# Kernel optimization log

Measured on AMD Instinct MI355X. Metric: run time of the kernel, lower is better.

The kernel has to match this reference:

```python
import jax, jax.numpy as jnp
import numpy as np

N_NODES = 100000
N_EDGES = 3200000
F_IN = 512
HIDDEN = 16
N_CLASSES = 32
DROPOUT = 0.5


def setup_inputs() -> dict:
    key = jax.random.key(0)
    k1, k2, k3, k4, k5, k6 = jax.random.split(key, 6)
    X = jax.random.normal(k1, (N_NODES, F_IN), dtype=jnp.float32)
    edge_src = jax.random.randint(k2, (N_EDGES,), 0, N_NODES, dtype=jnp.int32)
    edge_dst = jax.random.randint(k3, (N_EDGES,), 0, N_NODES, dtype=jnp.int32)
    # normalized adjacency values (positive, like D^-1/2 A D^-1/2 entries)
    edge_w = jax.random.uniform(k4, (N_EDGES,), dtype=jnp.float32)
    W1 = jax.random.normal(k5, (F_IN, HIDDEN), dtype=jnp.float32) * (1.0 / np.sqrt(F_IN))
    W2 = jax.random.normal(k6, (HIDDEN, N_CLASSES), dtype=jnp.float32) * (1.0 / np.sqrt(HIDDEN))
    return {"X": X, "edge_src": edge_src, "edge_dst": edge_dst,
            "edge_w": edge_w, "W1": W1, "W2": W2}


def _dropout(x, key, rate):
    keep = 1.0 - rate
    mask = jax.random.bernoulli(key, keep, x.shape)
    return jnp.where(mask, x / keep, jnp.zeros((), x.dtype))


def _spmm(h, edge_src, edge_dst, edge_w):
    # A @ h with A given as COO edge list: out[d] = sum_e w_e * h[s_e]
    msgs = h[edge_src] * edge_w[:, None]  # [E, C]
    return jax.ops.segment_sum(msgs, edge_dst, num_segments=h.shape[0])


def reference(X, edge_src, edge_dst, edge_w, W1, W2):
    key = jax.random.key(42)
    kd1, kd2 = jax.random.split(key)
    # layer 1: dropout -> GraphConv(relu)  (Spektral: act(A @ (X @ W)))
    H = _dropout(X, kd1, DROPOUT)
    H = H @ W1                                  # [N, HIDDEN]
    H = _spmm(H, edge_src, edge_dst, edge_w)    # [N, HIDDEN]
    H = jax.nn.relu(H)
    # layer 2: dropout -> GraphConv(softmax)
    H = _dropout(H, kd2, DROPOUT)
    H = H @ W2                                  # [N, N_CLASSES]
    H = _spmm(H, edge_src, edge_dst, edge_w)
    return jax.nn.softmax(H, axis=-1)
```

## Files before the change

### kernel.cpp

```cpp
#include <hip/hip_runtime.h>
#include <stdint.h>
#include <stddef.h>

#define N_NODES   100000
#define N_EDGES   3200000
#define F_IN      512
#define HIDDEN    16
#define N_CLASSES 32

#define BSHIFT 6
#define NBUK   ((N_NODES + 63) >> 6)
#define CAP    2368
#define TILE   8192
#define NB_BIN ((N_EDGES + TILE - 1) / TILE)
#define NW_MASK ((N_NODES * F_IN) / 32)
#define NB_MSK (NW_MASK / 256)
#define NB_G1  ((N_NODES + 63) / 64)

__host__ __device__ __forceinline__ uint32_t rotl32(uint32_t x, int r) {
#ifdef __HIP_DEVICE_COMPILE__
  return __builtin_amdgcn_alignbit(x, x, (uint32_t)(32 - r));
#else
  return (x << r) | (x >> (32 - r));
#endif
}

__host__ __device__ __forceinline__ void tf2x32_full(uint32_t k0, uint32_t k1,
                                                     uint32_t x0, uint32_t x1,
                                                     uint32_t* o0, uint32_t* o1) {
  const uint32_t k2 = k0 ^ k1 ^ 0x1BD11BDAu;
  x0 += k0; x1 += k1;
#define TF_R(r) { x0 += x1; x1 = rotl32(x1, (r)); x1 ^= x0; }
  TF_R(13) TF_R(15) TF_R(26) TF_R(6)   x0 += k1; x1 += k2 + 1u;
  TF_R(17) TF_R(29) TF_R(16) TF_R(24)  x0 += k2; x1 += k0 + 2u;
  TF_R(13) TF_R(15) TF_R(26) TF_R(6)   x0 += k0; x1 += k1 + 3u;
  TF_R(17) TF_R(29) TF_R(16) TF_R(24)  x0 += k1; x1 += k2 + 4u;
  TF_R(13) TF_R(15) TF_R(26) TF_R(6)   x0 += k2; x1 += k0 + 5u;
#undef TF_R
  *o0 = x0; *o1 = x1;
}

__device__ __forceinline__ bool keep_bit(uint32_t k0, uint32_t k1, uint32_t ctr) {
  uint32_t o0, o1;
  tf2x32_full(k0, k1, 0u, ctr, &o0, &o1);
  return (int32_t)(o0 ^ o1) >= 0;
}

__launch_bounds__(256)
__global__ void bin_mask_fused(const int* __restrict__ src, const int* __restrict__ dst,
                               const float* __restrict__ w, int* __restrict__ gcur,
                               int2* __restrict__ ep, uint32_t* __restrict__ mask1,
                               uint32_t kd0, uint32_t kd1) {
  __shared__ int lh[NBUK];
  __shared__ int gb[NBUK];
  const int tid = threadIdx.x;

  if (blockIdx.x < NB_BIN) {
    const int base = blockIdx.x * TILE;
    const int n = min(TILE, N_EDGES - base);

    for (int i = tid; i < NBUK; i += 256) lh[i] = 0;
    __syncthreads();

    for (int i = tid; i < n; i += 256)
      atomicAdd(&lh[dst[base + i] >> BSHIFT], 1);
    __syncthreads();

    for (int b = tid; b < NBUK; b += 256) {
      const int h = lh[b];
      gb[b] = h ? atomicAdd(&gcur[b], h) : 0;
      lh[b] = 0;
    }
    __syncthreads();

    for (int i = tid; i < n; i += 256) {
      const int e = base + i;
      const int d = dst[e];
      const int b = d >> BSHIFT;
      const int pos = gb[b] + atomicAdd(&lh[b], 1);
      if (pos < CAP)
        ep[(size_t)b * CAP + pos] =
            make_int2(src[e] | ((d & 63) << 17), __float_as_int(w[e]));
    }
    return;
  }

  const int mt = (blockIdx.x - NB_BIN) * 256 + tid;
  if (mt < NW_MASK) {
    const uint32_t base = (uint32_t)mt * 32u;
    uint32_t word = 0u;
#pragma unroll
    for (int j = 0; j < 32; j++) {
      uint32_t o0, o1;
      tf2x32_full(kd0, kd1, 0u, base + (uint32_t)j, &o0, &o1);
      word |= ((~(o0 ^ o1)) >> 31) << j;
    }
    mask1[mt] = word;
  }
}

__launch_bounds__(256)
__global__ void gemm1_mask(const float* __restrict__ X,
                           const float* __restrict__ W1,
                           const uint32_t* __restrict__ mask1,
                           float* __restrict__ H1) {
  __shared__ float W1s[F_IN * HIDDEN];
  const int tid = threadIdx.x;
  for (int i = tid; i < (F_IN * HIDDEN) / 4; i += 256) {
    const int f = i >> 2, m = i & 3;
    ((float4*)W1s)[f * 4 + (m ^ ((f >> 2) & 3))] = ((const float4*)W1)[i];
  }
  __syncthreads();

  const int p = tid & 3;
  const int node = blockIdx.x * 64 + (tid >> 2);
  if (node >= N_NODES) return;

  float acc[16];
#pragma unroll
  for (int j = 0; j < 16; j++) acc[j] = 0.0f;

  const float4* Xrow4 = (const float4*)(X + (size_t)node * F_IN);
  const uint32_t* Mrow = mask1 + (size_t)node * 16;
  const int sh0 = p << 2;
  const int sh1 = 16 + (p << 2);

  for (int it2 = 0; it2 < 16; ++it2) {
    const uint32_t mword = Mrow[it2];
    const float4 xv0 = Xrow4[it2 * 8 + p];
    const float4 xv1 = Xrow4[it2 * 8 + 4 + p];
    const uint32_t nib0 = mword >> sh0;
    const uint32_t nib1 = mword >> sh1;
    const float xs0[4] = {xv0.x, xv0.y, xv0.z, xv0.w};
    const float xs1[4] = {xv1.x, xv1.y, xv1.z, xv1.w};

#pragma unroll
    for (int e = 0; e < 4; e++) {
      const float xd = (nib0 >> e) & 1u ? xs0[e] + xs0[e] : 0.0f;
      const int f = it2 * 32 + p * 4 + e;
      const float4* row = (const float4*)&W1s[f * 16];
#pragma unroll
      for (int q = 0; q < 4; q++) {
        const float4 wv = row[q ^ p];
        acc[q * 4 + 0] += xd * wv.x;
        acc[q * 4 + 1] += xd * wv.y;
        acc[q * 4 + 2] += xd * wv.z;
        acc[q * 4 + 3] += xd * wv.w;
      }
    }
#pragma unroll
    for (int e = 0; e < 4; e++) {
      const float xd = (nib1 >> e) & 1u ? xs1[e] + xs1[e] : 0.0f;
      const int f = it2 * 32 + 16 + p * 4 + e;
      const float4* row = (const float4*)&W1s[f * 16];
#pragma unroll
      for (int q = 0; q < 4; q++) {
        const float4 wv = row[q ^ p];
        acc[q * 4 + 0] += xd * wv.x;
        acc[q * 4 + 1] += xd * wv.y;
        acc[q * 4 + 2] += xd * wv.z;
        acc[q * 4 + 3] += xd * wv.w;
      }
    }
  }

  float a2[8];
#pragma unroll
  for (int k = 0; k < 8; k++) {
    const float keep = (p & 2) ? acc[8 + k] : acc[k];
    const float send = (p & 2) ? acc[k]     : acc[8 + k];
    a2[k] = keep + __shfl_xor(send, 2);
  }
  float r0, r1, r2, r3;
  {
    const float k0v = (p & 1) ? a2[4] : a2[0];
    const float s0v = (p & 1) ? a2[0] : a2[4];
    r0 = k0v + __shfl_xor(s0v, 1);
    const float k1v = (p & 1) ? a2[5] : a2[1];
    const float s1v = (p & 1) ? a2[1] : a2[5];
    r1 = k1v + __shfl_xor(s1v, 1);
    const float k2v = (p & 1) ? a2[6] : a2[2];
    const float s2v = (p & 1) ? a2[2] : a2[6];
    r2 = k2v + __shfl_xor(s2v, 1);
    const float k3v = (p & 1) ? a2[7] : a2[3];
    const float s3v = (p & 1) ? a2[3] : a2[7];
    r3 = k3v + __shfl_xor(s3v, 1);
  }
  *(float4*)(H1 + (size_t)node * HIDDEN + p * 4) = make_float4(r0, r1, r2, r3);
}

__launch_bounds__(256)
__global__ void bucket_gather1(const int* __restrict__ gcur, const int2* __restrict__ ep,
                               const float* __restrict__ H1, float* __restrict__ H2d,
                               uint32_t k0, uint32_t k1) {
  __shared__ int2 B[CAP];
  __shared__ int lh[64], lex[64], lcur[64];
  const int tid = threadIdx.x;
  const int b = blockIdx.x;

  if (tid < 64) lh[tid] = 0;
  __syncthreads();

  const int c = min(gcur[b], CAP);
  const int2* ebase = ep + (size_t)b * CAP;

  for (int k = tid; k < c; k += 256)
    atomicAdd(&lh[(ebase[k].x >> 17) & 63], 1);
  __syncthreads();

  if (tid < 64) {
    const int v = lh[tid];
    int s = v;
    for (int off = 1; off < 64; off <<= 1) {
      const int t = __shfl_up(s, off);
      if (tid >= off) s += t;
    }
    lex[tid] = s - v;
    lcur[tid] = s - v;
  }
  __syncthreads();

  for (int k = tid; k < c; k += 256) {
    const int2 r = ebase[k];
    const int p = atomicAdd(&lcur[(r.x >> 17) & 63], 1);
    B[p] = r;
  }
  __syncthreads();

  const int lane = tid & 63, wid = tid >> 6;
  const int ei = lane >> 4, f = lane & 15;
  for (int ln = wid; ln < 64; ln += 4) {
    const int ng = (b << BSHIFT) + ln;
    if (ng >= N_NODES) break;
    const int beg = lex[ln], cnt = lh[ln];
    float acc = 0.0f;
    for (int k = beg + ei; k < beg + cnt; k += 4) {
      const int2 r = B[k];
      acc += __int_as_float(r.y) * H1[(size_t)(r.x & 0x1FFFF) * HIDDEN + f];
    }
    acc += __shfl_xor(acc, 16);
    acc += __shfl_xor(acc, 32);
    float v = fmaxf(acc, 0.0f);
    v = keep_bit(k0, k1, (uint32_t)ng * HIDDEN + (uint32_t)f) ? v * 2.0f : 0.0f;
    if (lane < 16) H2d[(size_t)ng * HIDDEN + f] = v;
  }
}

__launch_bounds__(256)
__global__ void bucket_gather2(const int* __restrict__ gcur, const int2* __restrict__ ep,
                               const float* __restrict__ H2d, const float* __restrict__ W2,
                               float* __restrict__ O) {
  __shared__ int2 B[CAP];
  __shared__ float W2s[HIDDEN][N_CLASSES];
  __shared__ int lh[64], lex[64], lcur[64];
  const int tid = threadIdx.x;
  const int b = blockIdx.x;

  if (tid < 64) lh[tid] = 0;
  for (int i = tid; i < HIDDEN * N_CLASSES; i += 256) ((float*)W2s)[i] = W2[i];
  __syncthreads();

  const int c = min(gcur[b], CAP);
  const int2* ebase = ep + (size_t)b * CAP;

  for (int k = tid; k < c; k += 256)
    atomicAdd(&lh[(ebase[k].x >> 17) & 63], 1);
  __syncthreads();

  if (tid < 64) {
    const int v = lh[tid];
    int s = v;
    for (int off = 1; off < 64; off <<= 1) {
      const int t = __shfl_up(s, off);
      if (tid >= off) s += t;
    }
    lex[tid] = s - v;
    lcur[tid] = s - v;
  }
  __syncthreads();

  for (int k = tid; k < c; k += 256) {
    const int2 r = ebase[k];
    const int p = atomicAdd(&lcur[(r.x >> 17) & 63], 1);
    B[p] = r;
  }
  __syncthreads();

  const int lane = tid & 63, wid = tid >> 6;
  const int ei = lane >> 4, f = lane & 15;
  const int cl = lane & 31;
  for (int ln = wid; ln < 64; ln += 4) {
    const int ng = (b << BSHIFT) + ln;
    if (ng >= N_NODES) break;
    const int beg = lex[ln], cnt = lh[ln];
    float acc = 0.0f;
    for (int k = beg + ei; k < beg + cnt; k += 4) {
      const int2 r = B[k];
      acc += __int_as_float(r.y) * H2d[(size_t)(r.x & 0x1FFFF) * HIDDEN + f];
    }
    acc += __shfl_xor(acc, 16);
    acc += __shfl_xor(acc, 32);
    float lg = 0.0f;
#pragma unroll
    for (int fq = 0; fq < HIDDEN; fq++)
      lg += __shfl(acc, fq) * W2s[fq][cl];
    float m = lg;
#pragma unroll
    for (int off = 16; off >= 1; off >>= 1) m = fmaxf(m, __shfl_xor(m, off));
    const float ex = __expf(lg - m);
    float ss = ex;
#pragma unroll
    for (int off = 16; off >= 1; off >>= 1) ss += __shfl_xor(ss, off);
    if (lane < 32) O[(size_t)ng * N_CLASSES + cl] = ex / ss;
  }
}

__launch_bounds__(256)
__global__ void gemm1_dropout_fb(const float* __restrict__ X,
                                 const float* __restrict__ W1,
                                 float* __restrict__ H1,
                                 uint32_t kd0, uint32_t kd1) {
  __shared__ float W1s[F_IN][HIDDEN];
  const int tid = threadIdx.x;
  for (int i = tid; i < (F_IN * HIDDEN) / 4; i += 256)
    ((float4*)W1s)[i] = ((const float4*)W1)[i];
  __syncthreads();
  const int n = blockIdx.x * 256 + tid;
  if (n >= N_NODES) return;
  float acc[HIDDEN];
#pragma unroll
  for (int j = 0; j < HIDDEN; j++) acc[j] = 0.0f;
  const float4* Xrow = (const float4*)(X + (size_t)n * F_IN);
  const uint32_t jbase = (uint32_t)n * F_IN;
  for (int cc = 0; cc < F_IN / 4; cc++) {
    float4 xv = Xrow[cc];
    float xs[4] = {xv.x, xv.y, xv.z, xv.w};
#pragma unroll
    for (int e = 0; e < 4; e++) {
      const int f = cc * 4 + e;
      const float x = keep_bit(kd0, kd1, jbase + (uint32_t)f) ? xs[e] * 2.0f : 0.0f;
      const float* wr = W1s[f];
#pragma unroll
      for (int j = 0; j < HIDDEN; j++) acc[j] += x * wr[j];
    }
  }
  float4* out = (float4*)(H1 + (size_t)n * HIDDEN);
#pragma unroll
  for (int q = 0; q < HIDDEN / 4; q++)
    out[q] = make_float4(acc[q * 4], acc[q * 4 + 1], acc[q * 4 + 2], acc[q * 4 + 3]);
}

__launch_bounds__(256)
__global__ void spmm1_atomic(const int* __restrict__ src, const int* __restrict__ dst,
                             const float* __restrict__ w, const float* __restrict__ H1,
                             float* __restrict__ H2) {
  const long long t = (long long)blockIdx.x * 256 + threadIdx.x;
  if (t >= (long long)N_EDGES * 4) return;
  const int e = (int)(t >> 2);
  const int q = (int)(t & 3);
  const float we = w[e];
  const float4 h = ((const float4*)(H1 + (size_t)src[e] * HIDDEN))[q];
  float* o = H2 + (size_t)dst[e] * HIDDEN + q * 4;
  unsafeAtomicAdd(o + 0, we * h.x);
  unsafeAtomicAdd(o + 1, we * h.y);
  unsafeAtomicAdd(o + 2, we * h.z);
  unsafeAtomicAdd(o + 3, we * h.w);
}

__launch_bounds__(256)
__global__ void gemm2_dropout(const float* __restrict__ H2,
                              const float* __restrict__ W2,
                              float* __restrict__ H3,
                              uint32_t kd0, uint32_t kd1) {
  __shared__ float W2s[HIDDEN][N_CLASSES];
  const int tid = threadIdx.x;
  for (int i = tid; i < (HIDDEN * N_CLASSES) / 4; i += 256)
    ((float4*)W2s)[i] = ((const float4*)W2)[i];
  __syncthreads();
  const int n = blockIdx.x * 256 + tid;
  if (n >= N_NODES) return;
  float acc[N_CLASSES];
#pragma unroll
  for (int j = 0; j < N_CLASSES; j++) acc[j] = 0.0f;
  const float4* hrow = (const float4*)(H2 + (size_t)n * HIDDEN);
  const uint32_t jbase = (uint32_t)n * HIDDEN;
#pragma unroll
  for (int qq = 0; qq < HIDDEN / 4; qq++) {
    float4 hv = hrow[qq];
    float hs[4] = {hv.x, hv.y, hv.z, hv.w};
#pragma unroll
    for (int e = 0; e < 4; e++) {
      const int cc = qq * 4 + e;
      float h = fmaxf(hs[e], 0.0f);
      h = keep_bit(kd0, kd1, jbase + (uint32_t)cc) ? h * 2.0f : 0.0f;
      const float* wr = W2s[cc];
#pragma unroll
      for (int j = 0; j < N_CLASSES; j++) acc[j] += h * wr[j];
    }
  }
  float4* out = (float4*)(H3 + (size_t)n * N_CLASSES);
#pragma unroll
  for (int q = 0; q < N_CLASSES / 4; q++)
    out[q] = make_float4(acc[q * 4], acc[q * 4 + 1], acc[q * 4 + 2], acc[q * 4 + 3]);
}

__launch_bounds__(256)
__global__ void spmm2_atomic(const int* __restrict__ src, const int* __restrict__ dst,
                             const float* __restrict__ w, const float* __restrict__ H3,
                             float* __restrict__ O) {
  const long long t = (long long)blockIdx.x * 256 + threadIdx.x;
  if (t >= (long long)N_EDGES * 8) return;
  const int e = (int)(t >> 3);
  const int q = (int)(t & 7);
  const float we = w[e];
  const float4 h = ((const float4*)(H3 + (size_t)src[e] * N_CLASSES))[q];
  float* o = O + (size_t)dst[e] * N_CLASSES + q * 4;
  unsafeAtomicAdd(o + 0, we * h.x);
  unsafeAtomicAdd(o + 1, we * h.y);
  unsafeAtomicAdd(o + 2, we * h.z);
  unsafeAtomicAdd(o + 3, we * h.w);
}

__launch_bounds__(256)
__global__ void softmax_rows(float* __restrict__ O) {
  const int n = blockIdx.x * 256 + threadIdx.x;
  if (n >= N_NODES) return;
  float4* row = (float4*)(O + (size_t)n * N_CLASSES);
  float v[N_CLASSES];
#pragma unroll
  for (int q = 0; q < N_CLASSES / 4; q++) {
    float4 t = row[q];
    v[q * 4 + 0] = t.x; v[q * 4 + 1] = t.y; v[q * 4 + 2] = t.z; v[q * 4 + 3] = t.w;
  }
  float m = v[0];
#pragma unroll
  for (int j = 1; j < N_CLASSES; j++) m = fmaxf(m, v[j]);
  float s = 0.0f;
#pragma unroll
  for (int j = 0; j < N_CLASSES; j++) { v[j] = __expf(v[j] - m); s += v[j]; }
  const float inv = 1.0f / s;
#pragma unroll
  for (int q = 0; q < N_CLASSES / 4; q++)
    row[q] = make_float4(v[q * 4] * inv, v[q * 4 + 1] * inv,
                         v[q * 4 + 2] * inv, v[q * 4 + 3] * inv);
}

extern "C" void kernel_launch(void* const* d_in, const int* in_sizes, int n_in,
                              void* d_out, int out_size, void* d_ws, size_t ws_size,
                              hipStream_t stream) {
  const float* X    = (const float*)d_in[0];
  const int*   esrc = (const int*)d_in[1];
  const int*   edst = (const int*)d_in[2];
  const float* ew   = (const float*)d_in[3];
  const float* W1   = (const float*)d_in[4];
  const float* W2   = (const float*)d_in[5];
  float* out = (float*)d_out;

  uint32_t kd1_0, kd1_1, kd2_0, kd2_1;
  tf2x32_full(0u, 42u, 0u, 0u, &kd1_0, &kd1_1);
  tf2x32_full(0u, 42u, 0u, 1u, &kd2_0, &kd2_1);

  const int nb_nodes = (N_NODES + 255) / 256;

  const size_t sz_ep  = (size_t)NBUK * CAP * sizeof(int2);
  const size_t sz_H1  = (size_t)N_NODES * HIDDEN * sizeof(float);
  const size_t sz_H2d = sz_H1;
  const size_t sz_mk  = (size_t)NW_MASK * sizeof(uint32_t);
  const size_t sz_cur = (size_t)NBUK * sizeof(int);
  const size_t need = sz_ep + sz_H1 + sz_H2d + sz_mk + sz_cur;

  char* p = (char*)d_ws;
  int2* ep = (int2*)p;       p += sz_ep;
  float* H1 = (float*)p;     p += sz_H1;
  float* H2d = (float*)p;    p += sz_H2d;
  uint32_t* mask1 = (uint32_t*)p; p += sz_mk;
  int* gcur = (int*)p;

  if (ws_size >= need) {
    hipMemsetAsync(gcur, 0, sz_cur, stream);
    bin_mask_fused<<<NB_BIN + NB_MSK, 256, 0, stream>>>(
        esrc, edst, ew, gcur, ep, mask1, kd1_0, kd1_1);
    gemm1_mask<<<NB_G1, 256, 0, stream>>>(X, W1, mask1, H1);
    bucket_gather1<<<NBUK, 256, 0, stream>>>(gcur, ep, H1, H2d, kd2_0, kd2_1);
    bucket_gather2<<<NBUK, 256, 0, stream>>>(gcur, ep, H2d, W2, out);
  } else {
    float* fH1 = (float*)d_ws;
    float* fH2 = fH1 + (size_t)N_NODES * HIDDEN;
    float* fH3 = fH2 + (size_t)N_NODES * HIDDEN;
    hipMemsetAsync(fH2, 0, (size_t)N_NODES * HIDDEN * sizeof(float), stream);
    hipMemsetAsync(out, 0, (size_t)out_size * sizeof(float), stream);
    gemm1_dropout_fb<<<nb_nodes, 256, 0, stream>>>(X, W1, fH1, kd1_0, kd1_1);
    spmm1_atomic<<<(N_EDGES * 4) / 256, 256, 0, stream>>>(esrc, edst, ew, fH1, fH2);
    gemm2_dropout<<<nb_nodes, 256, 0, stream>>>(fH2, W2, fH3, kd2_0, kd2_1);
    spmm2_atomic<<<(N_EDGES * 8) / 256, 256, 0, stream>>>(esrc, edst, ew, fH3, out);
    softmax_rows<<<nb_nodes, 256, 0, stream>>>(out);
  }
}
```

Before: 298.2 us.

## Move edge binning into GEMM1 kernel and process two nodes per thread

Dropout mask generation now runs in its own kernel, and edge binning moves into the GEMM1 kernel, with each block taking either a binning tile or a GEMM tile. The GEMM1 part now handles two nodes per thread (128 nodes per block), so every W1 value read from LDS is used twice. The aim is to overlap the memory-heavy binning with the compute-heavy GEMM and to cut LDS traffic per FMA. The cost is higher register pressure from two accumulator sets, and the ALU-bound mask generation no longer overlaps with binning.

```diff
diff --git a/kernel.cpp b/kernel.cpp
--- a/kernel.cpp
+++ b/kernel.cpp
@@ -15,7 +15,7 @@
 #define NB_BIN ((N_EDGES + TILE - 1) / TILE)
 #define NW_MASK ((N_NODES * F_IN) / 32)
 #define NB_MSK (NW_MASK / 256)
-#define NB_G1  ((N_NODES + 63) / 64)
+#define NB_G1M ((N_NODES + 127) / 128)
 
 __host__ __device__ __forceinline__ uint32_t rotl32(uint32_t x, int r) {
 #ifdef __HIP_DEVICE_COMPILE__
@@ -47,15 +47,34 @@
 }
 
 __launch_bounds__(256)
-__global__ void bin_mask_fused(const int* __restrict__ src, const int* __restrict__ dst,
-                               const float* __restrict__ w, int* __restrict__ gcur,
-                               int2* __restrict__ ep, uint32_t* __restrict__ mask1,
-                               uint32_t kd0, uint32_t kd1) {
-  __shared__ int lh[NBUK];
-  __shared__ int gb[NBUK];
+__global__ void mask_gen(uint32_t* __restrict__ mask1, uint32_t kd0, uint32_t kd1) {
+  const int mt = blockIdx.x * 256 + threadIdx.x;
+  if (mt >= NW_MASK) return;
+  const uint32_t base = (uint32_t)mt * 32u;
+  uint32_t word = 0u;
+#pragma unroll
+  for (int j = 0; j < 32; j++) {
+    uint32_t o0, o1;
+    tf2x32_full(kd0, kd1, 0u, base + (uint32_t)j, &o0, &o1);
+    word |= ((~(o0 ^ o1)) >> 31) << j;
+  }
+  mask1[mt] = word;
+}
+
+__launch_bounds__(256)
+__global__ void bin_gemm1_fused(const float* __restrict__ X,
+                                const float* __restrict__ W1,
+                                const uint32_t* __restrict__ mask1,
+                                float* __restrict__ H1,
+                                const int* __restrict__ src, const int* __restrict__ dst,
+                                const float* __restrict__ w, int* __restrict__ gcur,
+                                int2* __restrict__ ep) {
+  __shared__ __align__(16) float smem[F_IN * HIDDEN];
   const int tid = threadIdx.x;
 
   if (blockIdx.x < NB_BIN) {
+    int* lh = (int*)smem;
+    int* gb = (int*)smem + NBUK;
     const int base = blockIdx.x * TILE;
     const int n = min(TILE, N_EDGES - base);
 
@@ -85,27 +104,7 @@
     return;
   }
 
-  const int mt = (blockIdx.x - NB_BIN) * 256 + tid;
-  if (mt < NW_MASK) {
-    const uint32_t base = (uint32_t)mt * 32u;
-    uint32_t word = 0u;
-#pragma unroll
-    for (int j = 0; j < 32; j++) {
-      uint32_t o0, o1;
-      tf2x32_full(kd0, kd1, 0u, base + (uint32_t)j, &o0, &o1);
-      word |= ((~(o0 ^ o1)) >> 31) << j;
-    }
-    mask1[mt] = word;
-  }
-}
-
-__launch_bounds__(256)
-__global__ void gemm1_mask(const float* __restrict__ X,
-                           const float* __restrict__ W1,
-                           const uint32_t* __restrict__ mask1,
-                           float* __restrict__ H1) {
-  __shared__ float W1s[F_IN * HIDDEN];
-  const int tid = threadIdx.x;
+  float* W1s = smem;
   for (int i = tid; i < (F_IN * HIDDEN) / 4; i += 256) {
     const int f = i >> 2, m = i & 3;
     ((float4*)W1s)[f * 4 + (m ^ ((f >> 2) & 3))] = ((const float4*)W1)[i];
@@ -113,80 +112,96 @@
   __syncthreads();
 
   const int p = tid & 3;
-  const int node = blockIdx.x * 64 + (tid >> 2);
-  if (node >= N_NODES) return;
-
-  float acc[16];
-#pragma unroll
-  for (int j = 0; j < 16; j++) acc[j] = 0.0f;
-
-  const float4* Xrow4 = (const float4*)(X + (size_t)node * F_IN);
-  const uint32_t* Mrow = mask1 + (size_t)node * 16;
+  const int slot = tid >> 2;
+  const int nA = (blockIdx.x - NB_BIN) * 128 + slot;
+  const int nB = nA + 64;
+  const bool okA = nA < N_NODES, okB = nB < N_NODES;
+  const int nAc = okA ? nA : 0, nBc = okB ? nB : 0;
+
+  float accA[16], accB[16];
+#pragma unroll
+  for (int j = 0; j < 16; j++) { accA[j] = 0.0f; accB[j] = 0.0f; }
+
+  const float4* XA = (const float4*)(X + (size_t)nAc * F_IN);
+  const float4* XB = (const float4*)(X + (size_t)nBc * F_IN);
+  const uint32_t* MA = mask1 + (size_t)nAc * 16;
+  const uint32_t* MB = mask1 + (size_t)nBc * 16;
   const int sh0 = p << 2;
   const int sh1 = 16 + (p << 2);
 
   for (int it2 = 0; it2 < 16; ++it2) {
-    const uint32_t mword = Mrow[it2];
-    const float4 xv0 = Xrow4[it2 * 8 + p];
-    const float4 xv1 = Xrow4[it2 * 8 + 4 + p];
-    const uint32_t nib0 = mword >> sh0;
-    const uint32_t nib1 = mword >> sh1;
-    const float xs0[4] = {xv0.x, xv0.y, xv0.z, xv0.w};
-    const float xs1[4] = {xv1.x, xv1.y, xv1.z, xv1.w};
+    const uint32_t mwA = MA[it2], mwB = MB[it2];
+    const float4 xa0 = XA[it2 * 8 + p],     xa1 = XA[it2 * 8 + 4 + p];
+    const float4 xb0 = XB[it2 * 8 + p],     xb1 = XB[it2 * 8 + 4 + p];
+    const float a0[4] = {xa0.x, xa0.y, xa0.z, xa0.w};
+    const float a1[4] = {xa1.x, xa1.y, xa1.z, xa1.w};
+    const float b0[4] = {xb0.x, xb0.y, xb0.z, xb0.w};
+    const float b1[4] = {xb1.x, xb1.y, xb1.z, xb1.w};
 
 #pragma unroll
     for (int e = 0; e < 4; e++) {
-      const float xd = (nib0 >> e) & 1u ? xs0[e] + xs0[e] : 0.0f;
+      const float xdA = ((mwA >> (sh0 + e)) & 1u) ? a0[e] + a0[e] : 0.0f;
+      const float xdB = ((mwB >> (sh0 + e)) & 1u) ? b0[e] + b0[e] : 0.0f;
       const int f = it2 * 32 + p * 4 + e;
       const float4* row = (const float4*)&W1s[f * 16];
 #pragma unroll
       for (int q = 0; q < 4; q++) {
         const float4 wv = row[q ^ p];
-        acc[q * 4 + 0] += xd * wv.x;
-        acc[q * 4 + 1] += xd * wv.y;
-        acc[q * 4 + 2] += xd * wv.z;
-        acc[q * 4 + 3] += xd * wv.w;
+        accA[q * 4 + 0] += xdA * wv.x;  accB[q * 4 + 0] += xdB * wv.x;
+        accA[q * 4 + 1] += xdA * wv.y;  accB[q * 4 + 1] += xdB * wv.y;
+        accA[q * 4 + 2] += xdA * wv.z;  accB[q * 4 + 2] += xdB * wv.z;
+        accA[q * 4 + 3] += xdA * wv.w;  accB[q * 4 + 3] += xdB * wv.w;
       }
     }
 #pragma unroll
     for (int e = 0; e < 4; e++) {
-      const float xd = (nib1 >> e) & 1u ? xs1[e] + xs1[e] : 0.0f;
+      const float xdA = ((mwA >> (sh1 + e)) & 1u) ? a1[e] + a1[e] : 0.0f;
+      const float xdB = ((mwB >> (sh1 + e)) & 1u) ? b1[e] + b1[e] : 0.0f;
       const int f = it2 * 32 + 16 + p * 4 + e;
       const float4* row = (const float4*)&W1s[f * 16];
 #pragma unroll
       for (int q = 0; q < 4; q++) {
         const float4 wv = row[q ^ p];
-        acc[q * 4 + 0] += xd * wv.x;
-        acc[q * 4 + 1] += xd * wv.y;
-        acc[q * 4 + 2] += xd * wv.z;
-        acc[q * 4 + 3] += xd * wv.w;
+        accA[q * 4 + 0] += xdA * wv.x;  accB[q * 4 + 0] += xdB * wv.x;
+        accA[q * 4 + 1] += xdA * wv.y;  accB[q * 4 + 1] += xdB * wv.y;
+        accA[q * 4 + 2] += xdA * wv.z;  accB[q * 4 + 2] += xdB * wv.z;
+        accA[q * 4 + 3] += xdA * wv.w;  accB[q * 4 + 3] += xdB * wv.w;
       }
     }
   }
 
-  float a2[8];
-#pragma unroll
-  for (int k = 0; k < 8; k++) {
-    const float keep = (p & 2) ? acc[8 + k] : acc[k];
-    const float send = (p & 2) ? acc[k]     : acc[8 + k];
-    a2[k] = keep + __shfl_xor(send, 2);
-  }
-  float r0, r1, r2, r3;
-  {
-    const float k0v = (p & 1) ? a2[4] : a2[0];
-    const float s0v = (p & 1) ? a2[0] : a2[4];
-    r0 = k0v + __shfl_xor(s0v, 1);
-    const float k1v = (p & 1) ? a2[5] : a2[1];
-    const float s1v = (p & 1) ? a2[1] : a2[5];
-    r1 = k1v + __shfl_xor(s1v, 1);
-    const float k2v = (p & 1) ? a2[6] : a2[2];
-    const float s2v = (p & 1) ? a2[2] : a2[6];
-    r2 = k2v + __shfl_xor(s2v, 1);
-    const float k3v = (p & 1) ? a2[7] : a2[3];
-    const float s3v = (p & 1) ? a2[3] : a2[7];
-    r3 = k3v + __shfl_xor(s3v, 1);
-  }
-  *(float4*)(H1 + (size_t)node * HIDDEN + p * 4) = make_float4(r0, r1, r2, r3);
+#define CROSSP_REDUCE(ACC, OK, NODE)                                     \
+  {                                                                      \
+    float a2[8];                                                         \
+    _Pragma("unroll")                                                    \
+    for (int k = 0; k < 8; k++) {                                        \
+      const float keep = (p & 2) ? ACC[8 + k] : ACC[k];                  \
+      const float send = (p & 2) ? ACC[k]     : ACC[8 + k];              \
+      a2[k] = keep + __shfl_xor(send, 2);                                \
+    }                                                                    \
+    float r0, r1, r2, r3;                                                \
+    {                                                                    \
+      const float k0v = (p & 1) ? a2[4] : a2[0];                         \
+      const float s0v = (p & 1) ? a2[0] : a2[4];                         \
+      r0 = k0v + __shfl_xor(s0v, 1);                                     \
+      const float k1v = (p & 1) ? a2[5] : a2[1];                         \
+      const float s1v = (p & 1) ? a2[1] : a2[5];                         \
+      r1 = k1v + __shfl_xor(s1v, 1);                                     \
+      const float k2v = (p & 1) ? a2[6] : a2[2];                         \
+      const float s2v = (p & 1) ? a2[2] : a2[6];                         \
+      r2 = k2v + __shfl_xor(s2v, 1);                                     \
+      const float k3v = (p & 1) ? a2[7] : a2[3];                         \
+      const float s3v = (p & 1) ? a2[3] : a2[7];                         \
+      r3 = k3v + __shfl_xor(s3v, 1);                                     \
+    }                                                                    \
+    if (OK)                                                              \
+      *(float4*)(H1 + (size_t)(NODE) * HIDDEN + p * 4) =                 \
+          make_float4(r0, r1, r2, r3);                                   \
+  }
+
+  CROSSP_REDUCE(accA, okA, nA)
+  CROSSP_REDUCE(accB, okB, nB)
+#undef CROSSP_REDUCE
 }
 
 __launch_bounds__(256)
@@ -478,9 +493,9 @@
 
   if (ws_size >= need) {
     hipMemsetAsync(gcur, 0, sz_cur, stream);
-    bin_mask_fused<<<NB_BIN + NB_MSK, 256, 0, stream>>>(
-        esrc, edst, ew, gcur, ep, mask1, kd1_0, kd1_1);
-    gemm1_mask<<<NB_G1, 256, 0, stream>>>(X, W1, mask1, H1);
+    mask_gen<<<NB_MSK, 256, 0, stream>>>(mask1, kd1_0, kd1_1);
+    bin_gemm1_fused<<<NB_BIN + NB_G1M, 256, 0, stream>>>(
+        X, W1, mask1, H1, esrc, edst, ew, gcur, ep);
     bucket_gather1<<<NBUK, 256, 0, stream>>>(gcur, ep, H1, H2d, kd2_0, kd2_1);
     bucket_gather2<<<NBUK, 256, 0, stream>>>(gcur, ep, H2d, W2, out);
   } else {
```

Result: slower. 377.4 us (+26.6%).
